# Optimization experiments

Measured on AMD Instinct MI355X. Metric: run time of the kernel, lower is better.

## Reference

```python
import jax, jax.numpy as jnp
import numpy as np

B, N, D_MAX, D_LEN, D_MODEL, MODES, N_CLASS = 64, 128, 1024, 512, 512, 64, 1024


def setup_inputs() -> dict:
    key = jax.random.key(0)
    ks = jax.random.split(key, 8)
    s = 0.02
    return {
        "input_embedding": jax.random.normal(ks[0], (B, N, D_MAX), jnp.float32),
        "W_lin": jax.random.normal(ks[1], (D_LEN, D_MAX), jnp.float32) * s,
        "b_lin": jnp.zeros((D_LEN,), jnp.float32),
        "Wq": jax.random.normal(ks[2], (D_MODEL, D_LEN), jnp.float32) * s,
        "Wk": jax.random.normal(ks[3], (D_MODEL, D_LEN), jnp.float32) * s,
        "W_add": jax.random.normal(ks[4], (D_MODEL, D_LEN), jnp.float32) * s,
        "b_add": jnp.zeros((D_MODEL,), jnp.float32),
        "W_final": jax.random.normal(ks[5], (N_CLASS, D_MODEL * N), jnp.float32) * s,
        "b_final": jnp.zeros((N_CLASS,), jnp.float32),
    }


def reference(input_embedding, W_lin, b_lin, Wq, Wk, W_add, b_add, W_final, b_final):
    # d_max_len -> d_length projection
    e = input_embedding @ W_lin.T + b_lin            # [B, N, d_length]
    q = e @ Wq.T                                      # [B, N, d_model]
    k = e @ Wk.T                                      # [B, N, d_model]
    # h == 1 in the original, so [B,N,h,E] permutations collapse to [B,E,N]
    xq = jnp.swapaxes(q, 1, 2)                        # [B, E, N]
    xk = jnp.swapaxes(k, 1, 2)                        # [B, E, N]
    n = xq.shape[-1]
    modes = min(n // 2, MODES)                        # index_q = index_k_v = range(modes): contiguous prefix
    xq_ft = jnp.fft.rfft(xq, axis=-1)[..., :modes]    # [B, E, modes] complex64
    xk_ft = jnp.fft.rfft(xk, axis=-1)[..., :modes]    # [B, E, modes]
    # torch.einsum on complex does NOT conjugate; plain complex product, then complex tanh
    scores = jnp.tanh(jnp.einsum('bex,bey->bxy', xq_ft, xk_ft))   # [B, modes, modes]
    xqkv = jnp.einsum('bxy,bey->bex', scores, xk_ft)  # [B, E, modes]
    out_ft = jnp.zeros((xq.shape[0], xq.shape[1], n // 2 + 1), jnp.complex64)
    out_ft = out_ft.at[..., :modes].set(xqkv)
    out = jnp.fft.irfft(out_ft / (D_MODEL * D_MODEL), n=n, axis=-1)  # [B, E, N]
    out = jnp.swapaxes(out, 1, 2)                     # [B, N, E]
    out = out + (e @ W_add.T + b_add)                 # residual add path (dropout = identity at eval)
    out = out.reshape(out.shape[0], -1)               # [B, N*d_model]
    return out @ W_final.T + b_final                  # [B, number_class]
```

## Files before the change

kernel.cpp:

```cpp
#include <hip/hip_runtime.h>

typedef float f32x4 __attribute__((ext_vector_type(4)));
typedef __bf16 bf16x8 __attribute__((ext_vector_type(8)));
typedef unsigned short u16;

#define DEVFN __device__ __forceinline__

DEVFN u16 f2bf(float f) {
    unsigned u = __builtin_bit_cast(unsigned, f);
    u += 0x7fffu + ((u >> 16) & 1u);
    return (u16)(u >> 16);
}
DEVFN float bf2f(u16 h) {
    unsigned u = ((unsigned)h) << 16;
    return __builtin_bit_cast(float, u);
}

DEVFN void gl2lds16(const void* g, void* l) {
    __builtin_amdgcn_global_load_lds(
        (const __attribute__((address_space(1))) void*)g,
        (__attribute__((address_space(3))) void*)l, 16, 0, 0);
}

DEVFN void gemm_core128(const u16* __restrict__ Ab, int lda,
                        const u16* __restrict__ Bb, int ldb, int K,
                        u16* As, u16* Bs, f32x4 (&acc)[4][4], int tid) {
    const int wv = tid >> 6, ln = tid & 63;
    const int wm = (wv >> 1) * 64, wn = (wv & 1) * 64;
    for (int k0 = 0; k0 < K; k0 += 64) {
        #pragma unroll
        for (int i = 0; i < 4; i++) {
            int c = i * 256 + tid;
            int row = c >> 3, kp = (c & 7) * 8;
            gl2lds16(Ab + (long)row * lda + k0 + kp, &As[(i * 256 + wv * 64) * 8]);
        }
        #pragma unroll
        for (int i = 0; i < 4; i++) {
            int c = i * 256 + tid;
            int row = c >> 3, kp = (c & 7) * 8;
            gl2lds16(Bb + (long)row * ldb + k0 + kp, &Bs[(i * 256 + wv * 64) * 8]);
        }
        __syncthreads();
        #pragma unroll
        for (int kk = 0; kk < 2; kk++) {
            bf16x8 af[4], bfr[4];
            const int rr = ln & 15, ks = kk * 32 + (ln >> 4) * 8;
            #pragma unroll
            for (int m = 0; m < 4; m++) af[m] = *(const bf16x8*)&As[(wm + m * 16 + rr) * 64 + ks];
            #pragma unroll
            for (int n = 0; n < 4; n++) bfr[n] = *(const bf16x8*)&Bs[(wn + n * 16 + rr) * 64 + ks];
            #pragma unroll
            for (int m = 0; m < 4; m++)
                #pragma unroll
                for (int n = 0; n < 4; n++)
                    acc[m][n] = __builtin_amdgcn_mfma_f32_16x16x32_bf16(af[m], bfr[n], acc[m][n], 0, 0, 0);
        }
        __syncthreads();
    }
}

__global__ void k_wt(const float* __restrict__ Wlin, const float* __restrict__ Wq,
                     const float* __restrict__ Wk, const float* __restrict__ Wadd,
                     u16* __restrict__ Wlin_b, u16* __restrict__ Wcat_b,
                     u16* __restrict__ F2, u16* __restrict__ F2T, u16* __restrict__ G) {
    int bid = blockIdx.x;
    if (bid < 640) {
        long idx = ((long)bid * 256 + threadIdx.x) * 8;
        const float* src;
        u16* dst;
        long off;
        if (idx < 524288) { src = Wlin; dst = Wlin_b + idx; off = idx; }
        else {
            long r = idx - 524288;
            dst = Wcat_b + r;
            if (r < 262144)      { src = Wq;   off = r; }
            else if (r < 524288) { src = Wk;   off = r - 262144; }
            else                 { src = Wadd; off = r - 524288; }
        }
        float4 a = *(const float4*)&src[off];
        float4 b = *(const float4*)&src[off + 4];
        ushort4 r0 = { f2bf(a.x), f2bf(a.y), f2bf(a.z), f2bf(a.w) };
        ushort4 r1 = { f2bf(b.x), f2bf(b.y), f2bf(b.z), f2bf(b.w) };
        *(ushort4*)dst = r0;
        *(ushort4*)(dst + 4) = r1;
    } else {
        int t = (bid - 640) * 256 + threadIdx.x;
        int which = t >> 14;
        int r = (t >> 7) & 127, c = t & 127;
        const float TWO_PI_128 = 6.283185307179586f / 128.f;
        if (which == 0) {
            int m = r & 63;
            int ph = (m * c) & 127;
            float ang = (float)ph * TWO_PI_128;
            float v = (r < 64) ? cosf(ang) : -sinf(ang);
            u16 h = f2bf(v);
            F2[r * 128 + c] = h;
            F2T[c * 128 + r] = h;
        } else {
            int m = c & 63;
            int ph = (m * r) & 127;
            float ang = (float)ph * TWO_PI_128;
            float cm = (m == 0) ? 1.f : 2.f;
            const float s = 1.f / (128.f * 512.f * 512.f);
            float v = (c < 64) ? cm * s * cosf(ang) : -cm * s * sinf(ang);
            G[r * 128 + c] = f2bf(v);
        }
    }
}

__global__ __launch_bounds__(256)
void k_gemm_e(const float* __restrict__ X, const u16* __restrict__ Wb,
              const float* __restrict__ bias, u16* __restrict__ eb) {
    __shared__ __align__(16) u16 As[32 * 64];
    __shared__ __align__(16) u16 Bs[256 * 64];
    const int tid = threadIdx.x, wv = tid >> 6, ln = tid & 63;
    const int L = blockIdx.x;
    const int xcd = L & 7, j = L >> 3;
    const int m_idx = xcd * 32 + (j >> 1), xh = j & 1;
    const int m0 = m_idx * 32, n0 = xh * 256;
    f32x4 acc[2][4] = {};
    for (int k0 = 0; k0 < 1024; k0 += 64) {
        #pragma unroll
        for (int i = 0; i < 8; i++) {
            int c = i * 256 + tid;
            int row = c >> 3, kp = (c & 7) * 8;
            gl2lds16(Wb + (long)(n0 + row) * 1024 + k0 + kp, &Bs[(i * 256 + wv * 64) * 8]);
        }
        {
            int row = tid >> 3, colg = (tid & 7) * 8;
            const float4* src = (const float4*)&X[(long)(m0 + row) * 1024 + k0 + colg];
            float4 a = src[0], b = src[1];
            ushort4 r0 = { f2bf(a.x), f2bf(a.y), f2bf(a.z), f2bf(a.w) };
            ushort4 r1 = { f2bf(b.x), f2bf(b.y), f2bf(b.z), f2bf(b.w) };
            *(ushort4*)&As[row * 64 + colg] = r0;
            *(ushort4*)&As[row * 64 + colg + 4] = r1;
        }
        __syncthreads();
        #pragma unroll
        for (int kk = 0; kk < 2; kk++) {
            bf16x8 af[2], bfr[4];
            const int rr = ln & 15, ks = kk * 32 + (ln >> 4) * 8;
            #pragma unroll
            for (int m = 0; m < 2; m++) af[m] = *(const bf16x8*)&As[(m * 16 + rr) * 64 + ks];
            #pragma unroll
            for (int n = 0; n < 4; n++) bfr[n] = *(const bf16x8*)&Bs[(wv * 64 + n * 16 + rr) * 64 + ks];
            #pragma unroll
            for (int m = 0; m < 2; m++)
                #pragma unroll
                for (int n = 0; n < 4; n++)
                    acc[m][n] = __builtin_amdgcn_mfma_f32_16x16x32_bf16(af[m], bfr[n], acc[m][n], 0, 0, 0);
        }
        __syncthreads();
    }
    const int fq = ln >> 4, fr = ln & 15;
    #pragma unroll
    for (int m = 0; m < 2; m++)
        #pragma unroll
        for (int n = 0; n < 4; n++)
            #pragma unroll
            for (int j2 = 0; j2 < 4; j2++) {
                int row = m0 + m * 16 + fq * 4 + j2;
                int col = n0 + wv * 64 + n * 16 + fr;
                eb[(long)row * 512 + col] = f2bf(acc[m][n][j2] + bias[col]);
            }
}

__global__ __launch_bounds__(256)
void k_gemm_qka(const u16* __restrict__ A, const u16* __restrict__ B,
                u16* __restrict__ qg, u16* __restrict__ kg, u16* __restrict__ kT,
                u16* __restrict__ T, const float* __restrict__ bias) {
    __shared__ __align__(16) u16 As[128 * 64];
    __shared__ __align__(16) u16 Bs[128 * 64];
    const int tid = threadIdx.x, wv = tid >> 6, ln = tid & 63;
    int orig = blockIdx.y * 12 + blockIdx.x;
    int wg = (orig & 7) * 96 + (orig >> 3);
    const int by = wg / 12, bx = wg % 12;
    const u16* Ab = A + (long)(by * 128) * 512;
    const u16* Bb = B + (long)(bx * 128) * 512;
    f32x4 acc[4][4] = {};
    gemm_core128(Ab, 512, Bb, 512, 512, As, Bs, acc, tid);
    const int wm = (wv >> 1) * 64, wn = (wv & 1) * 64;
    const int fq = ln >> 4, fr = ln & 15;
    #pragma unroll
    for (int m = 0; m < 4; m++)
        #pragma unroll
        for (int n = 0; n < 4; n++) {
            int col = bx * 128 + wn + n * 16 + fr;
            int nn0 = wm + m * 16 + fq * 4;
            if (col < 512) {
                #pragma unroll
                for (int j = 0; j < 4; j++)
                    qg[(long)(by * 128 + nn0 + j) * 512 + col] = f2bf(acc[m][n][j]);
            } else if (col < 1024) {
                int e = col - 512;
                ushort4 pk = { f2bf(acc[m][n][0]), f2bf(acc[m][n][1]),
                               f2bf(acc[m][n][2]), f2bf(acc[m][n][3]) };
                *(ushort4*)&kT[(long)by * 65536 + (long)e * 128 + nn0] = pk;
                #pragma unroll
                for (int j = 0; j < 4; j++)
                    kg[(long)(by * 128 + nn0 + j) * 512 + e] = f2bf(acc[m][n][j]);
            } else {
                #pragma unroll
                for (int j = 0; j < 4; j++)
                    T[(long)(by * 128 + nn0 + j) * 512 + (col - 1024)] = f2bf(acc[m][n][j] + bias[col - 1024]);
            }
        }
}

template<bool AL, bool BL>
DEVFN void mm128(const u16* __restrict__ Ap, const u16* __restrict__ Bp,
                 f32x4 (&acc)[4][4], int wm, int wn, int rr, int kq) {
    #pragma unroll
    for (int s = 0; s < 4; s++) {
        int ks = s * 32 + kq;
        bf16x8 af[4], bfr[4];
        #pragma unroll
        for (int m = 0; m < 4; m++) {
            int r = wm + m * 16 + rr;
            af[m] = AL ? *(const bf16x8*)&Ap[r * 136 + ks] : *(const bf16x8*)&Ap[r * 128 + ks];
        }
        #pragma unroll
        for (int n = 0; n < 4; n++) {
            int r = wn + n * 16 + rr;
            bfr[n] = BL ? *(const bf16x8*)&Bp[r * 136 + ks] : *(const bf16x8*)&Bp[r * 128 + ks];
        }
        #pragma unroll
        for (int m = 0; m < 4; m++)
            #pragma unroll
            for (int n = 0; n < 4; n++)
                acc[m][n] = __builtin_amdgcn_mfma_f32_16x16x32_bf16(af[m], bfr[n], acc[m][n], 0, 0, 0);
    }
}

__global__ __launch_bounds__(256, 1)
void k_fourier(const u16* __restrict__ qg, const u16* __restrict__ kg,
               const u16* __restrict__ kTg, const u16* __restrict__ F2g,
               const u16* __restrict__ F2Tg, const u16* __restrict__ Gg,
               u16* __restrict__ T) {
    __shared__ __align__(16) u16 L[53760];
    const int tid = threadIdx.x, wv = tid >> 6, ln = tid & 63;
    const int b = blockIdx.x;
    const int wm = (wv >> 1) * 64, wn = (wv & 1) * 64;
    const int rr = ln & 15, kq = (ln >> 4) * 8;
    const int fq = ln >> 4, fr = ln & 15;
    const u16* qb = qg + (long)b * 65536;
    const u16* kb = kg + (long)b * 65536;

    f32x4 acc[4][4] = {};
    for (int t = 0; t < 8; ++t) {
        #pragma unroll
        for (int i = 0; i < 4; i++) {
            int c = i * 256 + tid;
            int row = c >> 3;
            int swz = ((c & 7) * 16) ^ ((row & 7) << 4);
            gl2lds16((const char*)qb + (long)row * 1024 + t * 128 + swz,
                     L + (i * 256 + wv * 64) * 8);
            gl2lds16((const char*)kb + (long)row * 1024 + t * 128 + swz,
                     L + 8192 + (i * 256 + wv * 64) * 8);
        }
        __syncthreads();
        const u16* qs = L;
        const u16* ks_ = L + 8192;
        #pragma unroll
        for (int kk = 0; kk < 2; kk++) {
            int ks = kk * 32 + kq;
            bf16x8 af[4], bfr[4];
            #pragma unroll
            for (int m = 0; m < 4; m++) {
                int r = wm + m * 16 + rr;
                af[m] = *(const bf16x8*)&qs[(r * 64 + ks) ^ ((rr & 7) << 3)];
            }
            #pragma unroll
            for (int n = 0; n < 4; n++) {
                int r = wn + n * 16 + rr;
                bfr[n] = *(const bf16x8*)&ks_[(r * 64 + ks) ^ ((rr & 7) << 3)];
            }
            #pragma unroll
            for (int m = 0; m < 4; m++)
                #pragma unroll
                for (int n = 0; n < 4; n++)
                    acc[m][n] = __builtin_amdgcn_mfma_f32_16x16x32_bf16(af[m], bfr[n], acc[m][n], 0, 0, 0);
        }
        __syncthreads();
    }
    u16* Mb = L + 35840;
    #pragma unroll
    for (int m = 0; m < 4; m++)
        #pragma unroll
        for (int n = 0; n < 4; n++)
            #pragma unroll
            for (int j = 0; j < 4; j++)
                Mb[(wm + m * 16 + fq * 4 + j) * 136 + wn + n * 16 + fr] = f2bf(acc[m][n][j]);
    __syncthreads();

    {
        f32x4 a2[4][4] = {};
        mm128<true, false>(Mb, F2g, a2, wm, wn, rr, kq);
        u16* Pt = L;
        #pragma unroll
        for (int m = 0; m < 4; m++)
            #pragma unroll
            for (int n = 0; n < 4; n++) {
                ushort4 pk = { f2bf(a2[m][n][0]), f2bf(a2[m][n][1]),
                               f2bf(a2[m][n][2]), f2bf(a2[m][n][3]) };
                *(ushort4*)&Pt[(wn + n * 16 + fr) * 136 + wm + m * 16 + fq * 4] = pk;
            }
    }
    __syncthreads();

    {
        f32x4 a3[4][4] = {};
        const u16* Pt = L;
        #pragma unroll
        for (int s = 0; s < 4; s++) {
            int ks = s * 32 + kq;
            bf16x8 af[4], bfr[4];
            #pragma unroll
            for (int m = 0; m < 4; m++) {
                int r = (wv >> 1) * 32 + (m & 1) * 16 + (m >> 1) * 64 + rr;
                af[m] = *(const bf16x8*)&F2g[r * 128 + ks];
            }
            #pragma unroll
            for (int n = 0; n < 4; n++) {
                int r = (wv & 1) * 32 + (n & 1) * 16 + (n >> 1) * 64 + rr;
                bfr[n] = *(const bf16x8*)&Pt[r * 136 + ks];
            }
            #pragma unroll
            for (int m = 0; m < 4; m++)
                #pragma unroll
                for (int n = 0; n < 4; n++)
                    a3[m][n] = __builtin_amdgcn_mfma_f32_16x16x32_bf16(af[m], bfr[n], a3[m][n], 0, 0, 0);
        }
        u16* Sc = L + 17920;
        const int xb0 = (wv >> 1) * 32, yb0 = (wv & 1) * 32;
        #pragma unroll
        for (int m = 0; m < 2; m++)
            #pragma unroll
            for (int n = 0; n < 2; n++)
                #pragma unroll
                for (int j = 0; j < 4; j++) {
                    int x = xb0 + m * 16 + fq * 4 + j;
                    int y = yb0 + n * 16 + fr;
                    float c00 = a3[m][n][j];
                    float c01 = a3[m][n + 2][j];
                    float c10 = a3[m + 2][n][j];
                    float c11 = a3[m + 2][n + 2][j];
                    float re = c00 - c11, im = c01 + c10;
                    float tr, ti;
                    float x2 = 2.f * re, y2 = 2.f * im;
                    if (fabsf(x2) > 40.f) {
                        tr = (re > 0.f) ? 1.f : -1.f;
                        ti = 0.f;
                    } else {
                        float ex = expf(x2);
                        float sh = 0.5f * (ex - 1.f / ex), ch = 0.5f * (ex + 1.f / ex);
                        float sn, cs;
                        __sincosf(y2, &sn, &cs);
                        float d = ch + cs;
                        if (d > 1e-12f) {
                            tr = sh / d;
                            ti = sn / d;
                        } else {
                            tr = (re > 0.f) ? 1.f : ((re < 0.f) ? -1.f : 0.f);
                            ti = 0.f;
                        }
                    }
                    Sc[x * 136 + y] = f2bf(tr);
                    Sc[x * 136 + 64 + y] = f2bf(-ti);
                    Sc[(64 + x) * 136 + y] = f2bf(ti);
                    Sc[(64 + x) * 136 + 64 + y] = f2bf(tr);
                }
    }
    __syncthreads();

    {
        f32x4 a4[4][4] = {};
        mm128<true, false>(L + 17920, F2Tg, a4, wm, wn, rr, kq);
        u16* Wt = L;
        #pragma unroll
        for (int m = 0; m < 4; m++)
            #pragma unroll
            for (int n = 0; n < 4; n++) {
                ushort4 pk = { f2bf(a4[m][n][0]), f2bf(a4[m][n][1]),
                               f2bf(a4[m][n][2]), f2bf(a4[m][n][3]) };
                *(ushort4*)&Wt[(wn + n * 16 + fr) * 136 + wm + m * 16 + fq * 4] = pk;
            }
    }
    __syncthreads();

    {
        f32x4 a5[4][4] = {};
        mm128<false, true>(Gg, L, a5, wm, wn, rr, kq);
        u16* H2 = L + 35840;
        #pragma unroll
        for (int m = 0; m < 4; m++)
            #pragma unroll
            for (int n = 0; n < 4; n++)
                #pragma unroll
                for (int j = 0; j < 4; j++)
                    H2[(wm + m * 16 + fq * 4 + j) * 136 + wn + n * 16 + fr] = f2bf(a5[m][n][j]);
    }
    __syncthreads();

    {
        const u16* H2 = L + 35840;
        const u16* kTb = kTg + (long)b * 65536;
        #pragma unroll
        for (int et = 0; et < 4; et++) {
            bf16x8 br[4][4];
            #pragma unroll
            for (int n = 0; n < 4; n++)
                #pragma unroll
                for (int s = 0; s < 4; s++)
                    br[n][s] = *(const bf16x8*)&kTb[(long)(et * 128 + wn + n * 16 + rr) * 128 + s * 32 + kq];
            f32x4 ag[4][4] = {};
            #pragma unroll
            for (int s = 0; s < 4; s++) {
                int ks = s * 32 + kq;
                bf16x8 af[4];
                #pragma unroll
                for (int m = 0; m < 4; m++)
                    af[m] = *(const bf16x8*)&H2[(wm + m * 16 + rr) * 136 + ks];
                #pragma unroll
                for (int m = 0; m < 4; m++)
                    #pragma unroll
                    for (int n = 0; n < 4; n++)
                        ag[m][n] = __builtin_amdgcn_mfma_f32_16x16x32_bf16(af[m], br[n][s], ag[m][n], 0, 0, 0);
            }
            #pragma unroll
            for (int m = 0; m < 4; m++)
                #pragma unroll
                for (int n = 0; n < 4; n++)
                    #pragma unroll
                    for (int j = 0; j < 4; j++) {
                        long idx = ((long)b * 128 + wm + m * 16 + fq * 4 + j) * 512 + et * 128 + wn + n * 16 + fr;
                        T[idx] = f2bf(bf2f(T[idx]) + ag[m][n][j]);
                    }
        }
    }
}

__global__ __launch_bounds__(256)
void gemm_final(const u16* __restrict__ T, const float* __restrict__ Wf, float* __restrict__ part) {
    __shared__ __align__(16) u16 As[64 * 64];
    __shared__ __align__(16) u16 Bs[64 * 64];
    const int tid = threadIdx.x, wv = tid >> 6, ln = tid & 63;
    int orig = blockIdx.y * 16 + blockIdx.x;
    int wg = (orig & 7) * 128 + (orig >> 3);
    const int yk = wg >> 4, xn = wg & 15;
    const int bn = xn * 64;
    const long kbase = (long)yk * 1024;
    const int wm = (wv >> 1) * 32, wn = (wv & 1) * 32;
    f32x4 acc[2][2] = {};
    for (int k0 = 0; k0 < 1024; k0 += 64) {
        float4 v[4];
        #pragma unroll
        for (int i = 0; i < 4; i++) {
            int idx = i * 256 + tid;
            int row = idx >> 4, kp = (idx & 15) * 4;
            v[i] = *(const float4*)&Wf[(long)(bn + row) * 65536 + kbase + k0 + kp];
        }
        #pragma unroll
        for (int i = 0; i < 2; i++) {
            int c = i * 256 + tid;
            int row = c >> 3, kp = (c & 7) * 8;
            gl2lds16(T + (long)row * 65536 + kbase + k0 + kp, &As[(i * 256 + wv * 64) * 8]);
        }
        #pragma unroll
        for (int i = 0; i < 4; i++) {
            int idx = i * 256 + tid;
            int row = idx >> 4, kp = (idx & 15) * 4;
            ushort4 r = { f2bf(v[i].x), f2bf(v[i].y), f2bf(v[i].z), f2bf(v[i].w) };
            *(ushort4*)&Bs[row * 64 + kp] = r;
        }
        __syncthreads();
        #pragma unroll
        for (int kk = 0; kk < 2; kk++) {
            bf16x8 af[2], bfr[2];
            const int rr = ln & 15, ks = kk * 32 + (ln >> 4) * 8;
            #pragma unroll
            for (int m = 0; m < 2; m++) af[m] = *(const bf16x8*)&As[(wm + m * 16 + rr) * 64 + ks];
            #pragma unroll
            for (int n = 0; n < 2; n++) bfr[n] = *(const bf16x8*)&Bs[(wn + n * 16 + rr) * 64 + ks];
            #pragma unroll
            for (int m = 0; m < 2; m++)
                #pragma unroll
                for (int n = 0; n < 2; n++)
                    acc[m][n] = __builtin_amdgcn_mfma_f32_16x16x32_bf16(af[m], bfr[n], acc[m][n], 0, 0, 0);
        }
        __syncthreads();
    }
    const int fq = ln >> 4, fr = ln & 15;
    #pragma unroll
    for (int m = 0; m < 2; m++)
        #pragma unroll
        for (int n = 0; n < 2; n++)
            #pragma unroll
            for (int j = 0; j < 4; j++) {
                int row = wm + m * 16 + fq * 4 + j;
                int col = bn + wn + n * 16 + fr;
                part[(long)yk * 65536 + (long)row * 1024 + col] = acc[m][n][j];
            }
}

__global__ void k_reduce(const float* __restrict__ part, const float* __restrict__ bias,
                         float* __restrict__ out) {
    int t = blockIdx.x * 256 + threadIdx.x;
    float s = bias[t & 1023];
    #pragma unroll 8
    for (int ch = 0; ch < 64; ch++) s += part[(long)ch * 65536 + t];
    out[t] = s;
}

static const size_t MB = 1048576;
static const size_t OFF_T    = 0;
static const size_t OFF_Q    = 8 * MB;
static const size_t OFF_K    = 16 * MB;
static const size_t OFF_KT   = 24 * MB;
static const size_t OFF_EB   = 32 * MB;
static const size_t OFF_WLIN = 40 * MB;
static const size_t OFF_WCAT = 41 * MB;
static const size_t OFF_F2   = 43 * MB;
static const size_t OFF_F2T  = 43 * MB + 32768;
static const size_t OFF_G    = 43 * MB + 65536;
static const size_t OFF_PART = 8 * MB;

extern "C" void kernel_launch(void* const* d_in, const int* in_sizes, int n_in,
                              void* d_out, int out_size, void* d_ws, size_t ws_size,
                              hipStream_t stream) {
    const float* X      = (const float*)d_in[0];
    const float* W_lin  = (const float*)d_in[1];
    const float* b_lin  = (const float*)d_in[2];
    const float* Wq     = (const float*)d_in[3];
    const float* Wk     = (const float*)d_in[4];
    const float* W_add  = (const float*)d_in[5];
    const float* b_add  = (const float*)d_in[6];
    const float* Wf     = (const float*)d_in[7];
    const float* b_fin  = (const float*)d_in[8];
    float* out = (float*)d_out;

    char* ws = (char*)d_ws;
    u16* T      = (u16*)(ws + OFF_T);
    u16* qg     = (u16*)(ws + OFF_Q);
    u16* kg     = (u16*)(ws + OFF_K);
    u16* kT     = (u16*)(ws + OFF_KT);
    u16* eb     = (u16*)(ws + OFF_EB);
    u16* Wlin_b = (u16*)(ws + OFF_WLIN);
    u16* Wcat_b = (u16*)(ws + OFF_WCAT);
    u16* F2     = (u16*)(ws + OFF_F2);
    u16* F2T    = (u16*)(ws + OFF_F2T);
    u16* G      = (u16*)(ws + OFF_G);
    float* part = (float*)(ws + OFF_PART);

    k_wt<<<768, 256, 0, stream>>>(W_lin, Wq, Wk, W_add, Wlin_b, Wcat_b, F2, F2T, G);
    k_gemm_e<<<512, 256, 0, stream>>>(X, Wlin_b, b_lin, eb);
    k_gemm_qka<<<dim3(12, 64), 256, 0, stream>>>(eb, Wcat_b, qg, kg, kT, T, b_add);
    k_fourier<<<64, 256, 0, stream>>>(qg, kg, kT, F2, F2T, G, T);
    gemm_final<<<dim3(16, 64), 256, 0, stream>>>(T, Wf, part);
    k_reduce<<<256, 256, 0, stream>>>(part, b_fin, out);
}
```

Before: 201.5 us.

## Split fused Fourier kernel into three kernels for more parallelism

The single 64-block Fourier kernel, which occupies only 64 CUs, is split into three kernels: a Q·K^T product over 128 blocks, a per-batch spectral chain that writes H2 to global memory, and a final H2·K^T accumulation into T over 256 blocks. The aim is to use more of the GPU's CUs for the heavy first and last GEMMs. The cost is two extra launches and global round trips for the M and H2 intermediates. The gemm_final block-to-XCD mapping is also changed so that blocks on the same XCD share K slices.

```diff
diff --git a/kernel.cpp b/kernel.cpp
--- a/kernel.cpp
+++ b/kernel.cpp
@@ -207,6 +207,59 @@
         }
 }
 
+__global__ __launch_bounds__(256)
+void k_M(const u16* __restrict__ qg, const u16* __restrict__ kg, u16* __restrict__ Mg) {
+    __shared__ __align__(16) u16 As[64 * 64];
+    __shared__ __align__(16) u16 Bs[128 * 64];
+    const int tid = threadIdx.x, wv = tid >> 6, ln = tid & 63;
+    const int b = blockIdx.x >> 1, h = blockIdx.x & 1;
+    const u16* qb = qg + (long)b * 65536 + (long)(h * 64) * 512;
+    const u16* kb = kg + (long)b * 65536;
+    const int wm = (wv >> 1) * 32, wn = (wv & 1) * 64;
+    f32x4 acc[2][4] = {};
+    for (int k0 = 0; k0 < 512; k0 += 64) {
+        #pragma unroll
+        for (int i = 0; i < 2; i++) {
+            int c = i * 256 + tid;
+            int row = c >> 3, kp = (c & 7) * 8;
+            gl2lds16(qb + (long)row * 512 + k0 + kp, &As[(i * 256 + wv * 64) * 8]);
+        }
+        #pragma unroll
+        for (int i = 0; i < 4; i++) {
+            int c = i * 256 + tid;
+            int row = c >> 3, kp = (c & 7) * 8;
+            gl2lds16(kb + (long)row * 512 + k0 + kp, &Bs[(i * 256 + wv * 64) * 8]);
+        }
+        __syncthreads();
+        #pragma unroll
+        for (int kk = 0; kk < 2; kk++) {
+            bf16x8 af[2], bfr[4];
+            const int rr = ln & 15, ks = kk * 32 + (ln >> 4) * 8;
+            #pragma unroll
+            for (int m = 0; m < 2; m++) af[m] = *(const bf16x8*)&As[(wm + m * 16 + rr) * 64 + ks];
+            #pragma unroll
+            for (int n = 0; n < 4; n++) bfr[n] = *(const bf16x8*)&Bs[(wn + n * 16 + rr) * 64 + ks];
+            #pragma unroll
+            for (int m = 0; m < 2; m++)
+                #pragma unroll
+                for (int n = 0; n < 4; n++)
+                    acc[m][n] = __builtin_amdgcn_mfma_f32_16x16x32_bf16(af[m], bfr[n], acc[m][n], 0, 0, 0);
+        }
+        __syncthreads();
+    }
+    const int fq = ln >> 4, fr = ln & 15;
+    #pragma unroll
+    for (int m = 0; m < 2; m++)
+        #pragma unroll
+        for (int n = 0; n < 4; n++)
+            #pragma unroll
+            for (int j = 0; j < 4; j++) {
+                int row = h * 64 + wm + m * 16 + fq * 4 + j;
+                int col = wn + n * 16 + fr;
+                Mg[(long)b * 16384 + (long)row * 128 + col] = f2bf(acc[m][n][j]);
+            }
+}
+
 template<bool AL, bool BL>
 DEVFN void mm128(const u16* __restrict__ Ap, const u16* __restrict__ Bp,
                  f32x4 (&acc)[4][4], int wm, int wn, int rr, int kq) {
@@ -232,65 +285,21 @@
     }
 }
 
-__global__ __launch_bounds__(256, 1)
-void k_fourier(const u16* __restrict__ qg, const u16* __restrict__ kg,
-               const u16* __restrict__ kTg, const u16* __restrict__ F2g,
-               const u16* __restrict__ F2Tg, const u16* __restrict__ Gg,
-               u16* __restrict__ T) {
+__global__ __launch_bounds__(256)
+void k_SH(const u16* __restrict__ Mg, const u16* __restrict__ F2g, const u16* __restrict__ F2Tg,
+          const u16* __restrict__ Gg, u16* __restrict__ H2g) {
     __shared__ __align__(16) u16 L[53760];
     const int tid = threadIdx.x, wv = tid >> 6, ln = tid & 63;
     const int b = blockIdx.x;
     const int wm = (wv >> 1) * 64, wn = (wv & 1) * 64;
     const int rr = ln & 15, kq = (ln >> 4) * 8;
     const int fq = ln >> 4, fr = ln & 15;
-    const u16* qb = qg + (long)b * 65536;
-    const u16* kb = kg + (long)b * 65536;
-
-    f32x4 acc[4][4] = {};
-    for (int t = 0; t < 8; ++t) {
-        #pragma unroll
-        for (int i = 0; i < 4; i++) {
-            int c = i * 256 + tid;
-            int row = c >> 3;
-            int swz = ((c & 7) * 16) ^ ((row & 7) << 4);
-            gl2lds16((const char*)qb + (long)row * 1024 + t * 128 + swz,
-                     L + (i * 256 + wv * 64) * 8);
-            gl2lds16((const char*)kb + (long)row * 1024 + t * 128 + swz,
-                     L + 8192 + (i * 256 + wv * 64) * 8);
-        }
-        __syncthreads();
-        const u16* qs = L;
-        const u16* ks_ = L + 8192;
-        #pragma unroll
-        for (int kk = 0; kk < 2; kk++) {
-            int ks = kk * 32 + kq;
-            bf16x8 af[4], bfr[4];
-            #pragma unroll
-            for (int m = 0; m < 4; m++) {
-                int r = wm + m * 16 + rr;
-                af[m] = *(const bf16x8*)&qs[(r * 64 + ks) ^ ((rr & 7) << 3)];
-            }
-            #pragma unroll
-            for (int n = 0; n < 4; n++) {
-                int r = wn + n * 16 + rr;
-                bfr[n] = *(const bf16x8*)&ks_[(r * 64 + ks) ^ ((rr & 7) << 3)];
-            }
-            #pragma unroll
-            for (int m = 0; m < 4; m++)
-                #pragma unroll
-                for (int n = 0; n < 4; n++)
-                    acc[m][n] = __builtin_amdgcn_mfma_f32_16x16x32_bf16(af[m], bfr[n], acc[m][n], 0, 0, 0);
-        }
-        __syncthreads();
-    }
+
     u16* Mb = L + 35840;
-    #pragma unroll
-    for (int m = 0; m < 4; m++)
-        #pragma unroll
-        for (int n = 0; n < 4; n++)
-            #pragma unroll
-            for (int j = 0; j < 4; j++)
-                Mb[(wm + m * 16 + fq * 4 + j) * 136 + wn + n * 16 + fr] = f2bf(acc[m][n][j]);
+    for (int c = tid; c < 2048; c += 256) {
+        int row = c >> 4, col = (c & 15) * 8;
+        *(bf16x8*)&Mb[row * 136 + col] = *(const bf16x8*)&Mg[(long)b * 16384 + (long)row * 128 + col];
+    }
     __syncthreads();
 
     {
@@ -391,53 +400,48 @@
     {
         f32x4 a5[4][4] = {};
         mm128<false, true>(Gg, L, a5, wm, wn, rr, kq);
-        u16* H2 = L + 35840;
         #pragma unroll
         for (int m = 0; m < 4; m++)
             #pragma unroll
             for (int n = 0; n < 4; n++)
                 #pragma unroll
                 for (int j = 0; j < 4; j++)
-                    H2[(wm + m * 16 + fq * 4 + j) * 136 + wn + n * 16 + fr] = f2bf(a5[m][n][j]);
+                    H2g[(long)b * 16384 + (long)(wm + m * 16 + fq * 4 + j) * 128 + wn + n * 16 + fr]
+                        = f2bf(a5[m][n][j]);
+    }
+}
+
+__global__ __launch_bounds__(256)
+void k_T(const u16* __restrict__ H2g, const u16* __restrict__ kTg, u16* __restrict__ T) {
+    __shared__ __align__(16) u16 Hs[128 * 136];
+    __shared__ __align__(16) u16 Bs[128 * 136];
+    const int tid = threadIdx.x, wv = tid >> 6, ln = tid & 63;
+    const int et = blockIdx.x, b = blockIdx.y;
+    const int wm = (wv >> 1) * 64, wn = (wv & 1) * 64;
+    const int rr = ln & 15, kq = (ln >> 4) * 8;
+    const int fq = ln >> 4, fr = ln & 15;
+
+    for (int c = tid; c < 2048; c += 256) {
+        int row = c >> 4, col = (c & 15) * 8;
+        *(bf16x8*)&Hs[row * 136 + col] = *(const bf16x8*)&H2g[(long)b * 16384 + (long)row * 128 + col];
+        *(bf16x8*)&Bs[row * 136 + col] =
+            *(const bf16x8*)&kTg[(long)b * 65536 + (long)(et * 128 + row) * 128 + col];
     }
     __syncthreads();
 
-    {
-        const u16* H2 = L + 35840;
-        const u16* kTb = kTg + (long)b * 65536;
-        #pragma unroll
-        for (int et = 0; et < 4; et++) {
-            bf16x8 br[4][4];
-            #pragma unroll
-            for (int n = 0; n < 4; n++)
-                #pragma unroll
-                for (int s = 0; s < 4; s++)
-                    br[n][s] = *(const bf16x8*)&kTb[(long)(et * 128 + wn + n * 16 + rr) * 128 + s * 32 + kq];
-            f32x4 ag[4][4] = {};
-            #pragma unroll
-            for (int s = 0; s < 4; s++) {
-                int ks = s * 32 + kq;
-                bf16x8 af[4];
-                #pragma unroll
-                for (int m = 0; m < 4; m++)
-                    af[m] = *(const bf16x8*)&H2[(wm + m * 16 + rr) * 136 + ks];
-                #pragma unroll
-                for (int m = 0; m < 4; m++)
-                    #pragma unroll
-                    for (int n = 0; n < 4; n++)
-                        ag[m][n] = __builtin_amdgcn_mfma_f32_16x16x32_bf16(af[m], br[n][s], ag[m][n], 0, 0, 0);
-            }
-            #pragma unroll
-            for (int m = 0; m < 4; m++)
-                #pragma unroll
-                for (int n = 0; n < 4; n++)
-                    #pragma unroll
-                    for (int j = 0; j < 4; j++) {
-                        long idx = ((long)b * 128 + wm + m * 16 + fq * 4 + j) * 512 + et * 128 + wn + n * 16 + fr;
-                        T[idx] = f2bf(bf2f(T[idx]) + ag[m][n][j]);
-                    }
-        }
-    }
+    f32x4 acc[4][4] = {};
+    mm128<true, true>(Hs, Bs, acc, wm, wn, rr, kq);
+    #pragma unroll
+    for (int m = 0; m < 4; m++)
+        #pragma unroll
+        for (int n = 0; n < 4; n++)
+            #pragma unroll
+            for (int j = 0; j < 4; j++) {
+                int row = wm + m * 16 + fq * 4 + j;
+                int col = et * 128 + wn + n * 16 + fr;
+                long idx = ((long)b * 128 + row) * 512 + col;
+                T[idx] = f2bf(bf2f(T[idx]) + acc[m][n][j]);
+            }
 }
 
 __global__ __launch_bounds__(256)
@@ -445,9 +449,9 @@
     __shared__ __align__(16) u16 As[64 * 64];
     __shared__ __align__(16) u16 Bs[64 * 64];
     const int tid = threadIdx.x, wv = tid >> 6, ln = tid & 63;
-    int orig = blockIdx.y * 16 + blockIdx.x;
-    int wg = (orig & 7) * 128 + (orig >> 3);
-    const int yk = wg >> 4, xn = wg & 15;
+    int d = blockIdx.y * 16 + blockIdx.x;
+    int xcd = d & 7, s = d >> 3;
+    const int yk = xcd * 8 + (s & 7), xn = s >> 3;
     const int bn = xn * 64;
     const long kbase = (long)yk * 1024;
     const int wm = (wv >> 1) * 32, wn = (wv & 1) * 32;
@@ -518,11 +522,13 @@
 static const size_t OFF_K    = 16 * MB;
 static const size_t OFF_KT   = 24 * MB;
 static const size_t OFF_EB   = 32 * MB;
-static const size_t OFF_WLIN = 40 * MB;
-static const size_t OFF_WCAT = 41 * MB;
-static const size_t OFF_F2   = 43 * MB;
-static const size_t OFF_F2T  = 43 * MB + 32768;
-static const size_t OFF_G    = 43 * MB + 65536;
+static const size_t OFF_MG   = 40 * MB;
+static const size_t OFF_H2   = 42 * MB;
+static const size_t OFF_WLIN = 44 * MB;
+static const size_t OFF_WCAT = 45 * MB;
+static const size_t OFF_F2   = 47 * MB;
+static const size_t OFF_F2T  = 47 * MB + 32768;
+static const size_t OFF_G    = 47 * MB + 65536;
 static const size_t OFF_PART = 8 * MB;
 
 extern "C" void kernel_launch(void* const* d_in, const int* in_sizes, int n_in,
@@ -545,6 +551,8 @@
     u16* kg     = (u16*)(ws + OFF_K);
     u16* kT     = (u16*)(ws + OFF_KT);
     u16* eb     = (u16*)(ws + OFF_EB);
+    u16* Mg     = (u16*)(ws + OFF_MG);
+    u16* H2g    = (u16*)(ws + OFF_H2);
     u16* Wlin_b = (u16*)(ws + OFF_WLIN);
     u16* Wcat_b = (u16*)(ws + OFF_WCAT);
     u16* F2     = (u16*)(ws + OFF_F2);
@@ -555,7 +563,9 @@
     k_wt<<<768, 256, 0, stream>>>(W_lin, Wq, Wk, W_add, Wlin_b, Wcat_b, F2, F2T, G);
     k_gemm_e<<<512, 256, 0, stream>>>(X, Wlin_b, b_lin, eb);
     k_gemm_qka<<<dim3(12, 64), 256, 0, stream>>>(eb, Wcat_b, qg, kg, kT, T, b_add);
-    k_fourier<<<64, 256, 0, stream>>>(qg, kg, kT, F2, F2T, G, T);
+    k_M<<<128, 256, 0, stream>>>(qg, kg, Mg);
+    k_SH<<<64, 256, 0, stream>>>(Mg, F2, F2T, G, H2g);
+    k_T<<<dim3(4, 64), 256, 0, stream>>>(H2g, kT, T);
     gemm_final<<<dim3(16, 64), 256, 0, stream>>>(T, Wf, part);
     k_reduce<<<256, 256, 0, stream>>>(part, b_fin, out);
 }
```

Measured after the change: 178.1 us. 1.13x faster.
